# Optimization experiments

Hardware: AMD Instinct MI355X
Metric: run time of the kernel (lower is better)

## Reference

```python
import jax, jax.numpy as jnp
import numpy as np

EMBED_DIM = 1024
NUM_HEADS = 16
HEAD_DIM = EMBED_DIM // NUM_HEADS


def setup_inputs() -> dict:
    key = jax.random.key(0)
    ks = jax.random.split(key, 11)
    B, S, E = 4, 2048, EMBED_DIM
    s = 1.0 / np.sqrt(E)
    return {
        "q": jax.random.normal(ks[0], (B, S, E), jnp.float32),
        "k": jax.random.normal(ks[1], (B, S, E), jnp.float32),
        "v": jax.random.normal(ks[2], (B, S, E), jnp.float32),
        "Wq": jax.random.uniform(ks[3], (E, E), jnp.float32, -s, s),
        "bq": jax.random.uniform(ks[4], (E,), jnp.float32, -s, s),
        "Wk": jax.random.uniform(ks[5], (E, E), jnp.float32, -s, s),
        "bk": jax.random.uniform(ks[6], (E,), jnp.float32, -s, s),
        "Wv": jax.random.uniform(ks[7], (E, E), jnp.float32, -s, s),
        "bv": jax.random.uniform(ks[8], (E,), jnp.float32, -s, s),
        "Wo": jax.random.uniform(ks[9], (E, E), jnp.float32, -s, s),
        "bo": jax.random.uniform(ks[10], (E,), jnp.float32, -s, s),
    }


def _split_heads(x):
    B, S, E = x.shape
    return x.reshape(B, S, NUM_HEADS, HEAD_DIM).transpose(0, 2, 1, 3)  # [B,H,S,D]


def reference(q, k, v, Wq, bq, Wk, bk, Wv, bv, Wo, bo):
    # torch Linear: x @ W.T + b
    Q = _split_heads(q @ Wq.T + bq)
    K = _split_heads(k @ Wk.T + bk)
    V = _split_heads(v @ Wv.T + bv)
    scale = 1.0 / jnp.sqrt(jnp.float32(HEAD_DIM))
    scores = jnp.einsum("bhqd,bhkd->bhqk", Q, K) * scale  # [B,H,S,S]
    weights = jax.nn.softmax(scores, axis=-1)
    ctx = jnp.einsum("bhqk,bhkd->bhqd", weights, V)
    B, H, S, D = ctx.shape
    merged = ctx.transpose(0, 2, 1, 3).reshape(B, S, H * D)
    out = merged @ Wo.T + bo
    return out, weights
```

## Files before the change

kernel.cpp:

```cpp
#include <hip/hip_runtime.h>
#include <hip/hip_bf16.h>

typedef __bf16 bf16x8 __attribute__((ext_vector_type(8)));
typedef __bf16 bf16x4 __attribute__((ext_vector_type(4)));
typedef float f32x4 __attribute__((ext_vector_type(4)));

constexpr size_t XQ_OFF = 0;
constexpr size_t WQ_OFF = 25165824;
constexpr size_t Q_OFF  = 29360128;
constexpr size_t KK_OFF = 37748736;
constexpr size_t VT_OFF = 46137344;
constexpr size_t CTX_OFF= 54525952;

__device__ __forceinline__ void gload16(const void* g, void* s) {
    __builtin_amdgcn_global_load_lds((__attribute__((address_space(1))) void*)g,
                                     (__attribute__((address_space(3))) void*)s, 16, 0, 0);
}
#define WAIT_VM0()   asm volatile("s_waitcnt vmcnt(0)" ::: "memory")
#define WAIT_VM4()   asm volatile("s_waitcnt vmcnt(4)" ::: "memory")
#define WAIT_VM8()   asm volatile("s_waitcnt vmcnt(8)" ::: "memory")
#define WAIT_LGKM0() asm volatile("s_waitcnt lgkmcnt(0)" ::: "memory")
#define BAR()        __builtin_amdgcn_s_barrier()

__global__ __launch_bounds__(256) void convert_k(
    const float* __restrict__ q, const float* __restrict__ k, const float* __restrict__ v,
    const float* __restrict__ Wq, const float* __restrict__ Wk, const float* __restrict__ Wv,
    const float* __restrict__ Wo, __bf16* __restrict__ ws) {
    int id = blockIdx.x * 256 + threadIdx.x;
    const int NX = 1048576;
    const int NW = 131072;
    const float* src; size_t dst; int local;
    if (id < 3 * NX) {
        int z = id / NX; local = id - z * NX;
        src = (z == 0) ? q : ((z == 1) ? k : v);
        dst = XQ_OFF + (size_t)z * 8388608;
    } else {
        int i2 = id - 3 * NX;
        int z = i2 / NW; local = i2 - z * NW;
        src = (z == 0) ? Wq : ((z == 1) ? Wk : ((z == 2) ? Wv : Wo));
        dst = WQ_OFF + (size_t)z * 1048576;
    }
    const float4* s4 = (const float4*)(src + (size_t)local * 8);
    float4 a = s4[0], b = s4[1];
    bf16x8 o;
    o[0]=(__bf16)a.x; o[1]=(__bf16)a.y; o[2]=(__bf16)a.z; o[3]=(__bf16)a.w;
    o[4]=(__bf16)b.x; o[5]=(__bf16)b.y; o[6]=(__bf16)b.z; o[7]=(__bf16)b.w;
    *(bf16x8*)(ws + dst + (size_t)local * 8) = o;
}

template<int MODE>
__global__ __launch_bounds__(256) void gemm_k(
    __bf16* __restrict__ ws,
    const float* __restrict__ bq, const float* __restrict__ bk,
    const float* __restrict__ bv, const float* __restrict__ bo,
    float* __restrict__ out) {
    const int K = 1024;
    unsigned n = blockIdx.x + 64u * (blockIdx.y + 8u * blockIdx.z);
    unsigned cpx = (MODE == 0) ? 192u : 64u;
    unsigned m_ = (n & 7u) * cpx + (n >> 3);
    unsigned bx = m_ & 63u;
    unsigned rest = m_ >> 6;
    unsigned by = rest & 7u;
    unsigned bz = rest >> 3;

    int z = (int)bz;
    const __bf16* A; const __bf16* Bm; const float* bias;
    if (MODE == 0) {
        A    = ws + XQ_OFF + (size_t)z * 8388608;
        Bm   = ws + WQ_OFF + (size_t)z * 1048576;
        bias = (z == 0) ? bq : ((z == 1) ? bk : bv);
    } else {
        A    = ws + CTX_OFF;
        Bm   = ws + WQ_OFF + (size_t)3 * 1048576;
        bias = bo;
    }
    int row0 = (int)bx * 128, col0 = (int)by * 128;
    __shared__ __align__(16) __bf16 As[2][128 * 32];
    __shared__ __align__(16) __bf16 Bs[2][128 * 32];
    int t = threadIdx.x, lane = t & 63, w = t >> 6;
    int wr = w >> 1, wc = w & 1;
    f32x4 acc[4][4];
#pragma unroll
    for (int i = 0; i < 4; ++i)
#pragma unroll
        for (int j = 0; j < 4; ++j) acc[i][j] = (f32x4){0.f, 0.f, 0.f, 0.f};

    auto stage = [&](int buf, int kt) {
#pragma unroll
        for (int i = 0; i < 2; ++i) {
            int e = ((i * 4 + w) * 64 + lane) * 8;
            int r = e >> 5, c = e & 31;
            gload16(A  + (size_t)(row0 + r) * K + kt + c, &As[buf][e]);
            gload16(Bm + (size_t)(col0 + r) * K + kt + c, &Bs[buf][e]);
        }
    };

    stage(0, 0);
    int cur = 0;
    for (int kt = 0; kt < K; kt += 32) {
        bool nx = kt + 32 < K;
        if (nx) { stage(cur ^ 1, kt + 32); WAIT_VM4(); }
        else    { WAIT_VM0(); }
        BAR();
        const __bf16* Ac = As[cur];
        const __bf16* Bc = Bs[cur];
        bf16x8 af[4], bfr[4];
#pragma unroll
        for (int f = 0; f < 4; ++f) {
            af[f]  = *(const bf16x8*)&Ac[(wr * 64 + f * 16 + (lane & 15)) * 32 + (lane >> 4) * 8];
            bfr[f] = *(const bf16x8*)&Bc[(wc * 64 + f * 16 + (lane & 15)) * 32 + (lane >> 4) * 8];
        }
#pragma unroll
        for (int fr = 0; fr < 4; ++fr)
#pragma unroll
            for (int fc = 0; fc < 4; ++fc)
                acc[fr][fc] = __builtin_amdgcn_mfma_f32_16x16x32_bf16(af[fr], bfr[fc], acc[fr][fc], 0, 0, 0);
        WAIT_LGKM0();
        BAR();
        cur ^= 1;
    }

    if (MODE == 0) {
        __bf16* dqk = ws + Q_OFF + (size_t)z * 8388608;
        __bf16* dvt = ws + VT_OFF;
#pragma unroll
        for (int fr = 0; fr < 4; ++fr)
#pragma unroll
            for (int fc = 0; fc < 4; ++fc)
#pragma unroll
                for (int r = 0; r < 4; ++r) {
                    int m = row0 + wr * 64 + fr * 16 + ((lane >> 4) << 2) + r;
                    int nn = col0 + wc * 64 + fc * 16 + (lane & 15);
                    float val = acc[fr][fc][r] + bias[nn];
                    int bb = m >> 11, s = m & 2047, h = nn >> 6, d = nn & 63;
                    size_t bh = (size_t)bb * 16 + h;
                    if (z < 2) dqk[bh * 131072 + (size_t)s * 64 + d] = (__bf16)val;
                    else       dvt[bh * 131072 + (size_t)d * 2048 + s] = (__bf16)val;
                }
    } else {
#pragma unroll
        for (int fr = 0; fr < 4; ++fr)
#pragma unroll
            for (int fc = 0; fc < 4; ++fc)
#pragma unroll
                for (int r = 0; r < 4; ++r) {
                    int m = row0 + wr * 64 + fr * 16 + ((lane >> 4) << 2) + r;
                    int nn = col0 + wc * 64 + fc * 16 + (lane & 15);
                    out[(size_t)m * 1024 + nn] = acc[fr][fc][r] + bias[nn];
                }
    }
}

__global__ __launch_bounds__(512) void rowsum_k(const __bf16* __restrict__ ws,
                                                float* __restrict__ rs_out) {
    unsigned n = blockIdx.x + 8u * blockIdx.y;
    unsigned m = (n & 7u) * 64u + (n >> 3);
    int bh = (int)(m >> 3);
    int q0 = (int)(m & 7u) * 256;
    const __bf16* Qb = ws + Q_OFF  + (size_t)bh * 131072;
    const __bf16* Kb = ws + KK_OFF + (size_t)bh * 131072;
    __shared__ __align__(16) __bf16 Ks[2][64 * 64];
    int t = threadIdx.x, lane = t & 63, w = t >> 6, g = lane >> 4;
    const float SCALE = 0.125f;

    bf16x8 aq[2][2];
#pragma unroll
    for (int f = 0; f < 2; ++f) {
        int qr = q0 + w * 32 + f * 16 + (lane & 15);
        aq[f][0] = *(const bf16x8*)&Qb[(size_t)qr * 64 + g * 8];
        aq[f][1] = *(const bf16x8*)&Qb[(size_t)qr * 64 + 32 + g * 8];
    }

    { int r = t >> 3, c8 = t & 7;
      gload16(Kb + (size_t)r * 64 + ((c8 ^ (r & 7)) << 3), &Ks[0][t * 8]); }
    WAIT_VM0(); BAR();

    float rs[8] = {0.f,0.f,0.f,0.f,0.f,0.f,0.f,0.f};
    int cur = 0;
    for (int kt = 0; kt < 2048; kt += 64) {
        bool nx = kt < 1984;
        if (nx) {
            int r = t >> 3, c8 = t & 7;
            gload16(Kb + (size_t)(kt + 64 + r) * 64 + ((c8 ^ (r & 7)) << 3), &Ks[cur ^ 1][t * 8]);
        }
        const __bf16* Kc = Ks[cur];
        __builtin_amdgcn_s_setprio(1);
#pragma unroll
        for (int kc = 0; kc < 4; ++kc) {
            int krow = kc * 16 + (lane & 15);
            bf16x8 b0 = *(const bf16x8*)((const char*)Kc + krow * 128 + ((g * 16) ^ ((krow & 7) << 4)));
            bf16x8 b1 = *(const bf16x8*)((const char*)Kc + krow * 128 + (((4 + g) * 16) ^ ((krow & 7) << 4)));
#pragma unroll
            for (int f = 0; f < 2; ++f) {
                f32x4 s = (f32x4){0.f, 0.f, 0.f, 0.f};
                s = __builtin_amdgcn_mfma_f32_16x16x32_bf16(aq[f][0], b0, s, 0, 0, 0);
                s = __builtin_amdgcn_mfma_f32_16x16x32_bf16(aq[f][1], b1, s, 0, 0, 0);
#pragma unroll
                for (int r4 = 0; r4 < 4; ++r4) rs[f * 4 + r4] += __expf(s[r4] * SCALE);
            }
        }
        __builtin_amdgcn_s_setprio(0);
        WAIT_LGKM0();
        if (nx) WAIT_VM0();
        BAR();
        cur ^= 1;
    }
#pragma unroll
    for (int msk = 1; msk < 16; msk <<= 1)
#pragma unroll
        for (int i = 0; i < 8; ++i) rs[i] += __shfl_xor(rs[i], msk);
    if ((lane & 15) == 0) {
#pragma unroll
        for (int f = 0; f < 2; ++f)
#pragma unroll
            for (int r4 = 0; r4 < 4; ++r4)
                rs_out[(size_t)bh * 2048 + q0 + w * 32 + f * 16 + g * 4 + r4] = rs[f * 4 + r4];
    }
}

__global__ __launch_bounds__(512) void attnw_k(const __bf16* __restrict__ ws,
                                               const float* __restrict__ rsf,
                                               __bf16* __restrict__ wsw,
                                               float* __restrict__ wout) {
    unsigned n = blockIdx.x + 8u * blockIdx.y;
    unsigned m = (n & 7u) * 64u + (n >> 3);
    int bh = (int)(m >> 3);
    int q0 = (int)(m & 7u) * 256;

    const __bf16* Qb = ws + Q_OFF  + (size_t)bh * 131072;
    const __bf16* Kb = ws + KK_OFF + (size_t)bh * 131072;
    const __bf16* Vb = ws + VT_OFF + (size_t)bh * 131072;
    __bf16* ctx = wsw + CTX_OFF;

    int t = threadIdx.x, lane = t & 63, w = t >> 6, g = lane >> 4, q = lane & 15;
    __shared__ __align__(16) __bf16 Ks[2][64 * 64];
    __shared__ __align__(16) __bf16 Vts[2][64 * 64];
    __shared__ __align__(16) float Pf[128 * 64];
    const float SCALE = 0.125f;

    bf16x8 aq[2][2];
#pragma unroll
    for (int f = 0; f < 2; ++f) {
        int qr = q0 + w * 32 + f * 16 + q;
        aq[f][0] = *(const bf16x8*)&Qb[(size_t)qr * 64 + g * 8];
        aq[f][1] = *(const bf16x8*)&Qb[(size_t)qr * 64 + 32 + g * 8];
    }
    float rinv[2];
#pragma unroll
    for (int f = 0; f < 2; ++f)
        rinv[f] = 1.f / rsf[(size_t)bh * 2048 + q0 + w * 32 + f * 16 + q];

    { int r = t >> 3, c8 = t & 7;
      gload16(Kb + (size_t)r * 64   + ((c8 ^ (r & 7)) << 3), &Ks[0][t * 8]);
      gload16(Vb + (size_t)r * 2048 + ((c8 ^ (r & 7)) << 3), &Vts[0][t * 8]); }
    WAIT_VM0(); BAR();

    f32x4 cacc[2][4];
#pragma unroll
    for (int f = 0; f < 2; ++f)
#pragma unroll
        for (int dc = 0; dc < 4; ++dc) cacc[f][dc] = (f32x4){0.f, 0.f, 0.f, 0.f};

    int cur = 0;
    for (int kt = 0; kt < 2048; kt += 64) {
        bool nx = kt < 1984;
        if (nx) {
            int r = t >> 3, c8 = t & 7;
            gload16(Kb + (size_t)(kt + 64 + r) * 64 + ((c8 ^ (r & 7)) << 3), &Ks[cur ^ 1][t * 8]);
            gload16(Vb + (size_t)r * 2048 + (kt + 64) + ((c8 ^ (r & 7)) << 3), &Vts[cur ^ 1][t * 8]);
        }
        const __bf16* Kc = Ks[cur];
        const __bf16* Vc = Vts[cur];

        int2 pk[2][4];
#pragma unroll
        for (int f = 0; f < 2; ++f) {
#pragma unroll
            for (int kc = 0; kc < 4; ++kc) {
                int krow = kc * 16 + q;
                bf16x8 b0 = *(const bf16x8*)((const char*)Kc + krow * 128 + ((g * 16) ^ ((krow & 7) << 4)));
                bf16x8 b1 = *(const bf16x8*)((const char*)Kc + krow * 128 + (((4 + g) * 16) ^ ((krow & 7) << 4)));
                f32x4 s = (f32x4){0.f, 0.f, 0.f, 0.f};
                s = __builtin_amdgcn_mfma_f32_16x16x32_bf16(b0, aq[f][0], s, 0, 0, 0);
                s = __builtin_amdgcn_mfma_f32_16x16x32_bf16(b1, aq[f][1], s, 0, 0, 0);
                f32x4 e4;
#pragma unroll
                for (int r4 = 0; r4 < 4; ++r4) e4[r4] = __expf(s[r4] * SCALE) * rinv[f];
                int row_l = w * 16 + q;
                int c_l = (kc * 4 + g) ^ (row_l & 7);
                *(f32x4*)&Pf[row_l * 64 + c_l * 4] = e4;
                bf16x4 p4;
#pragma unroll
                for (int r4 = 0; r4 < 4; ++r4) p4[r4] = (__bf16)e4[r4];
                pk[f][kc] = __builtin_bit_cast(int2, p4);
            }
            WAIT_LGKM0(); BAR();
#pragma unroll
            for (int i = 0; i < 4; ++i) {
                int idx = t + 512 * i;
                int row128 = idx >> 4, c16 = idx & 15;
                int pc = c16 ^ (row128 & 7);
                f32x4 v = *(const f32x4*)&Pf[row128 * 64 + pc * 4];
                int grow = q0 + (row128 >> 4) * 32 + f * 16 + (row128 & 15);
                float* dst = wout + ((size_t)bh * 2048 + grow) * 2048 + kt + c16 * 4;
                *(f32x4*)dst = v;
            }
            BAR();
        }

        int src0 = q + ((lane & 16) << 1);
        int src1 = src0 + 16;
        bool hi = lane >= 32;
        __builtin_amdgcn_s_setprio(1);
#pragma unroll
        for (int f = 0; f < 2; ++f) {
#pragma unroll
            for (int ks = 0; ks < 2; ++ks) {
                int2 A0 = pk[f][2 * ks], A1 = pk[f][2 * ks + 1];
                int l0a = __shfl(A0.x, src0), l0b = __shfl(A1.x, src0);
                int l1a = __shfl(A0.y, src0), l1b = __shfl(A1.y, src0);
                int h0a = __shfl(A0.x, src1), h0b = __shfl(A1.x, src1);
                int h1a = __shfl(A0.y, src1), h1b = __shfl(A1.y, src1);
                int4 ai;
                ai.x = hi ? l0b : l0a;
                ai.y = hi ? l1b : l1a;
                ai.z = hi ? h0b : h0a;
                ai.w = hi ? h1b : h1a;
                bf16x8 ap = __builtin_bit_cast(bf16x8, ai);
#pragma unroll
                for (int dc = 0; dc < 4; ++dc) {
                    int vrow = dc * 16 + q;
                    bf16x8 bv = *(const bf16x8*)((const char*)Vc + vrow * 128 + ((ks * 64 + g * 16) ^ ((vrow & 7) << 4)));
                    cacc[f][dc] = __builtin_amdgcn_mfma_f32_16x16x32_bf16(ap, bv, cacc[f][dc], 0, 0, 0);
                }
            }
        }
        __builtin_amdgcn_s_setprio(0);
        WAIT_LGKM0();
        if (nx) { WAIT_VM8(); BAR(); }
        cur ^= 1;
    }

    int bb = bh >> 4, h = bh & 15;
#pragma unroll
    for (int f = 0; f < 2; ++f)
#pragma unroll
        for (int dc = 0; dc < 4; ++dc)
#pragma unroll
            for (int r4 = 0; r4 < 4; ++r4) {
                int qg = q0 + w * 32 + f * 16 + (g << 2) + r4;
                int d = dc * 16 + q;
                ctx[((size_t)bb * 2048 + qg) * 1024 + h * 64 + d] = (__bf16)cacc[f][dc][r4];
            }
}

extern "C" void kernel_launch(void* const* d_in, const int* in_sizes, int n_in,
                              void* d_out, int out_size, void* d_ws, size_t ws_size,
                              hipStream_t stream) {
    const float* q  = (const float*)d_in[0];
    const float* k  = (const float*)d_in[1];
    const float* v  = (const float*)d_in[2];
    const float* Wq = (const float*)d_in[3];
    const float* bq = (const float*)d_in[4];
    const float* Wk = (const float*)d_in[5];
    const float* bk = (const float*)d_in[6];
    const float* Wv = (const float*)d_in[7];
    const float* bv = (const float*)d_in[8];
    const float* Wo = (const float*)d_in[9];
    const float* bo = (const float*)d_in[10];
    __bf16* ws = (__bf16*)d_ws;
    float* out  = (float*)d_out;
    float* wout = out + 8388608;
    float* rsum = (float*)d_ws;

    convert_k<<<dim3(14336), dim3(256), 0, stream>>>(q, k, v, Wq, Wk, Wv, Wo, ws);
    gemm_k<0><<<dim3(64, 8, 3), dim3(256), 0, stream>>>(ws, bq, bk, bv, bo, out);
    rowsum_k<<<dim3(8, 64), dim3(512), 0, stream>>>(ws, rsum);
    attnw_k<<<dim3(8, 64), dim3(512), 0, stream>>>(ws, rsum, ws, wout);
    gemm_k<1><<<dim3(64, 8, 1), dim3(256), 0, stream>>>(ws, bq, bk, bv, bo, out);
}
```

Baseline: 493.9 us.

## Stage attention weights as bf16 in LDS and write all rows once per tile

The probability tile is now staged in shared memory as bf16 instead of fp32, so all 256 query rows fit and are written to the weights output in a single pass per key tile. This replaces two barrier-separated store phases with one. The K fragment loads are hoisted out of the f loop so they are reused across both row fragments. The emitted weights are now bf16-rounded values expanded back to fp32, which loses precision in the returned attention weights relative to the previous fp32 staging.

Result: slower. 518.7 us (+5.0%).

```diff
diff --git a/kernel.cpp b/kernel.cpp
--- a/kernel.cpp
+++ b/kernel.cpp
@@ -235,7 +235,7 @@
     int t = threadIdx.x, lane = t & 63, w = t >> 6, g = lane >> 4, q = lane & 15;
     __shared__ __align__(16) __bf16 Ks[2][64 * 64];
     __shared__ __align__(16) __bf16 Vts[2][64 * 64];
-    __shared__ __align__(16) float Pf[128 * 64];
+    __shared__ __align__(16) __bf16 Pf[256 * 64];
     const float SCALE = 0.125f;
 
     bf16x8 aq[2][2];
@@ -273,39 +273,46 @@
         const __bf16* Vc = Vts[cur];
 
         int2 pk[2][4];
-#pragma unroll
-        for (int f = 0; f < 2; ++f) {
-#pragma unroll
-            for (int kc = 0; kc < 4; ++kc) {
-                int krow = kc * 16 + q;
-                bf16x8 b0 = *(const bf16x8*)((const char*)Kc + krow * 128 + ((g * 16) ^ ((krow & 7) << 4)));
-                bf16x8 b1 = *(const bf16x8*)((const char*)Kc + krow * 128 + (((4 + g) * 16) ^ ((krow & 7) << 4)));
+        __builtin_amdgcn_s_setprio(1);
+#pragma unroll
+        for (int kc = 0; kc < 4; ++kc) {
+            int krow = kc * 16 + q;
+            bf16x8 b0 = *(const bf16x8*)((const char*)Kc + krow * 128 + ((g * 16) ^ ((krow & 7) << 4)));
+            bf16x8 b1 = *(const bf16x8*)((const char*)Kc + krow * 128 + (((4 + g) * 16) ^ ((krow & 7) << 4)));
+#pragma unroll
+            for (int f = 0; f < 2; ++f) {
                 f32x4 s = (f32x4){0.f, 0.f, 0.f, 0.f};
                 s = __builtin_amdgcn_mfma_f32_16x16x32_bf16(b0, aq[f][0], s, 0, 0, 0);
                 s = __builtin_amdgcn_mfma_f32_16x16x32_bf16(b1, aq[f][1], s, 0, 0, 0);
-                f32x4 e4;
-#pragma unroll
-                for (int r4 = 0; r4 < 4; ++r4) e4[r4] = __expf(s[r4] * SCALE) * rinv[f];
-                int row_l = w * 16 + q;
-                int c_l = (kc * 4 + g) ^ (row_l & 7);
-                *(f32x4*)&Pf[row_l * 64 + c_l * 4] = e4;
                 bf16x4 p4;
 #pragma unroll
-                for (int r4 = 0; r4 < 4; ++r4) p4[r4] = (__bf16)e4[r4];
-                pk[f][kc] = __builtin_bit_cast(int2, p4);
+                for (int r4 = 0; r4 < 4; ++r4)
+                    p4[r4] = (__bf16)(__expf(s[r4] * SCALE) * rinv[f]);
+                int2 pki = __builtin_bit_cast(int2, p4);
+                pk[f][kc] = pki;
+                int row_l = w * 32 + f * 16 + q;
+                int cw = (kc * 4 + g) ^ (row_l & 7);
+                *(int2*)((char*)Pf + row_l * 128 + cw * 8) = pki;
             }
-            WAIT_LGKM0(); BAR();
-#pragma unroll
-            for (int i = 0; i < 4; ++i) {
-                int idx = t + 512 * i;
-                int row128 = idx >> 4, c16 = idx & 15;
-                int pc = c16 ^ (row128 & 7);
-                f32x4 v = *(const f32x4*)&Pf[row128 * 64 + pc * 4];
-                int grow = q0 + (row128 >> 4) * 32 + f * 16 + (row128 & 15);
-                float* dst = wout + ((size_t)bh * 2048 + grow) * 2048 + kt + c16 * 4;
-                *(f32x4*)dst = v;
-            }
-            BAR();
+        }
+        __builtin_amdgcn_s_setprio(0);
+        WAIT_LGKM0();
+        __builtin_amdgcn_sched_barrier(0);
+        BAR();
+
+#pragma unroll
+        for (int i = 0; i < 8; ++i) {
+            int idx = t + 512 * i;
+            int r = idx >> 4, u = idx & 15;
+            int cu_ = u ^ (r & 7);
+            int2 d = *(const int2*)((const char*)Pf + r * 128 + cu_ * 8);
+            f32x4 v;
+            v[0] = __builtin_bit_cast(float, d.x << 16);
+            v[1] = __builtin_bit_cast(float, d.x & (int)0xffff0000);
+            v[2] = __builtin_bit_cast(float, d.y << 16);
+            v[3] = __builtin_bit_cast(float, d.y & (int)0xffff0000);
+            float* dst = wout + ((size_t)bh * 2048 + q0 + r) * 2048 + kt + u * 4;
+            *(f32x4*)dst = v;
         }
 
         int src0 = q + ((lane & 16) << 1);
```
